# Kernel tuning notes

Hardware: AMD Instinct MI355X
Metric: run time of the kernel (lower is better)

## Reference

```python
import jax, jax.numpy as jnp
import numpy as np

N = 100000      # total nodes across batch of graphs
E = 1600000     # total edges (avg degree 16)
DIN = 16        # raw node feature dim
H = 128         # social_hidden_dim
HEADS = 4
DOUT = H // HEADS
LAYERS = 2
G = 64          # number of graphs in batch
FOUT = 256      # fusion_hidden_dim
NEG_SLOPE = 0.2


def layer_norm(x, g, b, eps=1e-5):
    mu = x.mean(-1, keepdims=True)
    var = ((x - mu) ** 2).mean(-1, keepdims=True)
    return (x - mu) / jnp.sqrt(var + eps) * g + b


def gat_conv(h, src, dst, W, a_src, a_dst, bias):
    # h: [N,H]; src/dst: [E+N] (self-loops included)
    hp = (h @ W).reshape(N, HEADS, DOUT)                    # [N,heads,dout]
    al_s = jnp.einsum('nhd,hd->nh', hp, a_src)              # [N,heads]
    al_d = jnp.einsum('nhd,hd->nh', hp, a_dst)
    logits = jax.nn.leaky_relu(al_s[src] + al_d[dst], NEG_SLOPE)  # [Etot,heads]
    m = jax.ops.segment_max(logits, dst, num_segments=N)    # segment softmax over dst
    e = jnp.exp(logits - m[dst])
    denom = jax.ops.segment_sum(e, dst, num_segments=N)
    alpha = e / (denom[dst] + 1e-16)                        # [Etot,heads]
    msg = hp[src] * alpha[:, :, None]                       # [Etot,heads,dout]
    out = jax.ops.segment_sum(msg, dst, num_segments=N)     # scatter-add
    return out.reshape(N, H) + bias


def setup_inputs():
    key = jax.random.key(0)
    ks = jax.random.split(key, 24)
    s = 0.05
    inp = {
        'x': jax.random.normal(ks[0], (N, DIN), jnp.float32),
        'edge_index': jax.random.randint(ks[1], (2, E), 0, N, jnp.int32),
        'node2graph': (jnp.arange(N, dtype=jnp.int32) * G // N).astype(jnp.int32),
        'Wp': jax.random.normal(ks[2], (DIN, H)) * s,
        'bp': jnp.zeros((H,)),
        'Wq1': jax.random.normal(ks[3], (2 * H, H)) * s,
        'bq1': jnp.zeros((H,)),
        'gq': jnp.ones((H,)), 'beq': jnp.zeros((H,)),
        'Wq2': jax.random.normal(ks[4], (H, FOUT)) * s,
        'bq2': jnp.zeros((FOUT,)),
    }
    for i in range(LAYERS):
        inp[f'Wg{i}'] = jax.random.normal(ks[5 + 4 * i], (H, H)) * s
        inp[f'as{i}'] = jax.random.normal(ks[6 + 4 * i], (HEADS, DOUT)) * s
        inp[f'ad{i}'] = jax.random.normal(ks[7 + 4 * i], (HEADS, DOUT)) * s
        inp[f'bg{i}'] = jnp.zeros((H,))
        inp[f'g{i}'] = jnp.ones((H,))
        inp[f'be{i}'] = jnp.zeros((H,))
    return inp


def reference(x, edge_index, node2graph, Wp, bp, Wq1, bq1, gq, beq, Wq2, bq2,
              Wg0, as0, ad0, bg0, g0, be0, Wg1, as1, ad1, bg1, g1, be1):
    loop = jnp.arange(N, dtype=edge_index.dtype)
    src = jnp.concatenate([edge_index[0], loop])  # add self-loops (PyG default)
    dst = jnp.concatenate([edge_index[1], loop])

    h = jax.nn.gelu(x @ Wp + bp, approximate=False)
    params = [(Wg0, as0, ad0, bg0, g0, be0), (Wg1, as1, ad1, bg1, g1, be1)]
    for (W, a_s, a_d, b, g, be) in params:
        h_new = gat_conv(h, src, dst, W, a_s, a_d, b)
        h = layer_norm(h_new + h, g, be)  # dims match -> residual

    counts = jax.ops.segment_sum(jnp.ones((N, 1), h.dtype), node2graph, num_segments=G)
    mean_pool = jax.ops.segment_sum(h, node2graph, num_segments=G) / jnp.maximum(counts, 1.0)
    max_pool = jax.ops.segment_max(h, node2graph, num_segments=G)
    emb = jnp.concatenate([mean_pool, max_pool], axis=-1)  # [G, 2H]

    p = layer_norm(emb @ Wq1 + bq1, gq, beq)
    p = jax.nn.gelu(p, approximate=False)
    return p @ Wq2 + bq2  # [G, FOUT]
```

## Files before the change

kernel.cpp:

```cpp
#include <hip/hip_runtime.h>

typedef unsigned short u16;
typedef unsigned char u8;
typedef unsigned int u32;
typedef unsigned long long u64;
typedef short short8 __attribute__((ext_vector_type(8)));
typedef float f32x4 __attribute__((ext_vector_type(4)));
typedef float f32x2 __attribute__((ext_vector_type(2)));

#define NN   100000
#define EE   1600000
#define ETOT (EE + NN)
#define NG   64
#define WSTR 136
#define SCANB 98
#define NB   98
#define BCAP 24576
#define OCAP 262144
#define EPB  4096

constexpr size_t AL256(size_t x) { return (x + 255) & ~(size_t)255; }
constexpr size_t OFF_FLAG   = 0;
constexpr size_t OFF_BSUM   = AL256(OFF_FLAG + 256);
constexpr size_t OFF_BCNT   = AL256(OFF_BSUM + 128 * 4);
constexpr size_t OFF_ROWPTR = AL256(OFF_BCNT + 128 * 4);
constexpr size_t OFF_DEG    = AL256(OFF_ROWPTR + (size_t)(NN + 1) * 4);
constexpr size_t OFF_COL    = AL256(OFF_DEG + (size_t)NN * 4);
constexpr size_t OFF_ALS    = AL256(OFF_COL + (size_t)ETOT * 4);
constexpr size_t OFF_ALD    = AL256(OFF_ALS + (size_t)NN * 4 * 4);
constexpr size_t OFF_GSUM   = AL256(OFF_ALD + (size_t)NN * 4 * 4);
constexpr size_t OFF_GKEY   = AL256(OFF_GSUM + (size_t)NG * 128 * 4);
constexpr size_t OFF_GCNT   = AL256(OFF_GKEY + (size_t)NG * 128 * 4);
constexpr size_t OFF_H      = AL256(OFF_GCNT + (size_t)NG * 4);
constexpr size_t OFF_HPB    = AL256(OFF_H + (size_t)NN * 128 * 2);
constexpr size_t OFF_EBUF   = AL256(OFF_HPB + (size_t)NN * 128 * 1);
constexpr size_t OFF_OBUF   = AL256(OFF_EBUF + (size_t)NB * BCAP * 4);
constexpr size_t WS_TOTAL   = AL256(OFF_OBUF + (size_t)OCAP * 8);

__device__ u64 g_ws[WS_TOTAL / 8];

__device__ __forceinline__ char* wsp() { return (char*)g_ws; }
#define WS_FLAG   ((int*)(wsp() + OFF_FLAG))
#define WS_BSUM   ((int*)(wsp() + OFF_BSUM))
#define WS_BCNT   ((int*)(wsp() + OFF_BCNT))
#define WS_ROWPTR ((int*)(wsp() + OFF_ROWPTR))
#define WS_DEG    ((int*)(wsp() + OFF_DEG))
#define WS_COL    ((int*)(wsp() + OFF_COL))
#define WS_ALS    ((float*)(wsp() + OFF_ALS))
#define WS_ALD    ((float*)(wsp() + OFF_ALD))
#define WS_GSUM   ((float*)(wsp() + OFF_GSUM))
#define WS_GKEY   ((u32*)(wsp() + OFF_GKEY))
#define WS_GCNT   ((int*)(wsp() + OFF_GCNT))
#define WS_H      ((u16*)(wsp() + OFF_H))
#define WS_HPB    ((u8*)(wsp() + OFF_HPB))
#define WS_EBUF   ((u32*)(wsp() + OFF_EBUF))
#define WS_OBUF   ((u64*)(wsp() + OFF_OBUF))

__device__ __forceinline__ float b2f(u16 u) { return __uint_as_float(((u32)u) << 16); }
__device__ __forceinline__ float b2f_lo(u32 u) { return __uint_as_float(u << 16); }
__device__ __forceinline__ float b2f_hi(u32 u) { return __uint_as_float(u & 0xffff0000u); }
__device__ __forceinline__ u16 f2bf(float f) {
    u32 u = __float_as_uint(f);
    return (u16)((u + 0x7fffu + ((u >> 16) & 1u)) >> 16);
}
__device__ __forceinline__ float ldf(const void* p, int i, int bf) {
    return bf ? b2f(((const u16*)p)[i]) : ((const float*)p)[i];
}
__device__ __forceinline__ int ldint(const int* p, long long i, int wide) {
    return wide ? p[i * 2] : p[(size_t)i];
}
__device__ __forceinline__ u32 fkey(float f) {
    u32 u = __float_as_uint(f);
    return (u >> 31) ? ~u : (u | 0x80000000u);
}
__device__ __forceinline__ float funkey(u32 k) {
    u32 u = (k & 0x80000000u) ? (k & 0x7fffffffu) : ~k;
    return __uint_as_float(u);
}

__global__ __launch_bounds__(256) void k_zero(const void* __restrict__ x,
                                              const int* __restrict__ ei) {
    if (blockIdx.x == 0 && threadIdx.x < 64) {
        int t = threadIdx.x;
        const u16* p = (const u16*)x;
        u16 u = p[t * 2];
        int e = (u >> 7) & 0xff;
        int ok = ((u & 0x7fffu) == 0) || (e >= 0x60 && e <= 0x9f);
        u64 m1 = __ballot(ok);
        int z = (ei[t * 2 + 1] == 0);
        u64 m2 = __ballot(z);
        if (t == 0) {
            WS_FLAG[0] = (__popcll(m1) >= 48) ? 1 : 0;
            WS_FLAG[1] = (__popcll(m2) >= 56) ? 1 : 0;
        }
    }
    if (blockIdx.x == 0 && threadIdx.x == 64) WS_FLAG[2] = 0;
    int i = blockIdx.x * 256 + threadIdx.x;
    if (i < NN) WS_DEG[i] = 0;
    if (i < NG * 128) { WS_GSUM[i] = 0.f; WS_GKEY[i] = 0u; }
    if (i < NG) WS_GCNT[i] = 0;
    if (i < NB) WS_BCNT[i] = 0;
}

__global__ __launch_bounds__(256) void k_bucket(const int* __restrict__ ei) {
    __shared__ int lcnt[NB], lbase[NB], lcur[NB];
    int t = threadIdx.x;
    int wide = WS_FLAG[1];
    for (int i = t; i < NB; i += 256) { lcnt[i] = 0; lcur[i] = 0; }
    __syncthreads();
    int e0 = blockIdx.x * EPB + t;
    int sA[16], dA[16];
#pragma unroll
    for (int j = 0; j < 16; j++) {
        int e = e0 + j * 256;
        int s = -1, d = 0;
        if (e < ETOT) {
            if (e < EE) {
                if (wide) { s = ((const int2*)ei)[e].x; d = ((const int2*)ei)[(size_t)EE + e].x; }
                else      { s = ei[e];                  d = ei[(size_t)EE + e]; }
            } else { s = e - EE; d = s; }
            if ((u32)s >= NN || (u32)d >= NN) s = -1;
        }
        sA[j] = s; dA[j] = d;
        if (s >= 0) atomicAdd(&lcnt[d >> 10], 1);
    }
    __syncthreads();
    for (int i = t; i < NB; i += 256)
        lbase[i] = atomicAdd(&WS_BCNT[i], lcnt[i]);
    __syncthreads();
    u32* ebuf = WS_EBUF;
#pragma unroll
    for (int j = 0; j < 16; j++) {
        int s = sA[j], d = dA[j];
        if (s < 0) continue;
        int b = d >> 10;
        int r = atomicAdd(&lcur[b], 1);
        int slot = lbase[b] + r;
        if (slot < BCAP) {
            ebuf[(size_t)b * BCAP + slot] = ((u32)(d & 1023) << 17) | (u32)s;
        } else {
            int o = atomicAdd(&WS_FLAG[2], 1);
            if (o < OCAP) {
                WS_OBUF[o] = ((u64)(u32)d << 32) | (u32)s;
                atomicAdd(&WS_DEG[d], 1);
            }
        }
    }
}

__global__ __launch_bounds__(1024) void k_scan1() {
    __shared__ int hist[1024];
    __shared__ int wsum[16];
    int b = blockIdx.x, t = threadIdx.x;
    hist[t] = 0;
    __syncthreads();
    int bc = WS_BCNT[b]; if (bc > BCAP) bc = BCAP;
    const u32* eb = WS_EBUF + (size_t)b * BCAP;
    for (int i = t; i < bc; i += 1024)
        atomicAdd(&hist[eb[i] >> 17], 1);
    __syncthreads();
    int i = b * 1024 + t;
    int v = (i < NN) ? (WS_DEG[i] + hist[t]) : 0;
    int lane = t & 63, wv = t >> 6;
    int x = v;
#pragma unroll
    for (int off = 1; off < 64; off <<= 1) {
        int y = __shfl_up(x, off);
        if (lane >= off) x += y;
    }
    if (lane == 63) wsum[wv] = x;
    __syncthreads();
    if (wv == 0 && lane < 16) {
        int y = wsum[lane];
#pragma unroll
        for (int off = 1; off < 16; off <<= 1) {
            int z = __shfl_up(y, off);
            if (lane >= off) y += z;
        }
        wsum[lane] = y;
    }
    __syncthreads();
    int incl = x + (wv > 0 ? wsum[wv - 1] : 0);
    if (i < NN) WS_ROWPTR[i] = incl - v;
    if (t == 1023) WS_BSUM[b] = incl;
}

__global__ __launch_bounds__(256) void k_place() {
    __shared__ int cur[1024];
    __shared__ int sb[128];
    __shared__ int w0tot;
    int b = blockIdx.x, t = threadIdx.x;
    int lane = t & 63;
    if (t < 128) {
        int x = (t < SCANB) ? WS_BSUM[t] : 0;
#pragma unroll
        for (int off = 1; off < 64; off <<= 1) {
            int y = __shfl_up(x, off);
            if (lane >= off) x += y;
        }
        if (t == 63) w0tot = x;
        sb[t] = x;
    }
    __syncthreads();
    if (t >= 64 && t < 128) sb[t] += w0tot;
    __syncthreads();
    int add = (b > 0) ? sb[b - 1] : 0;
    int n0 = b << 10;
    for (int i = t; i < 1024; i += 256) {
        int n = n0 + i;
        int r = 0;
        if (n < NN) {
            r = WS_ROWPTR[n] + add;
            WS_ROWPTR[n] = r;
        }
        cur[i] = r;
    }
    if (b == 0 && t == 0) WS_ROWPTR[NN] = sb[127];
    __syncthreads();
    int bc = WS_BCNT[b]; if (bc > BCAP) bc = BCAP;
    const u32* eb = WS_EBUF + (size_t)b * BCAP;
    for (int i = t; i < bc; i += 256) {
        u32 pk = eb[i];
        int dl = pk >> 17, s = (int)(pk & 0x1ffffu);
        int pos = atomicAdd(&cur[dl], 1);
        WS_COL[pos] = s;
    }
    int cnt = WS_FLAG[2]; if (cnt > OCAP) cnt = OCAP;
    for (int i = t; i < cnt; i += 256) {
        u64 pk = WS_OBUF[i];
        int d = (int)(pk >> 32);
        if ((d >> 10) == b) {
            int pos = atomicAdd(&cur[d & 1023], 1);
            WS_COL[pos] = (int)(pk & 0xffffffffu);
        }
    }
}

__global__ __launch_bounds__(128) void k_proj(const void* __restrict__ x,
                                              const void* __restrict__ Wp,
                                              const void* __restrict__ bp) {
    __shared__ float sW[16 * 128];
    int t = threadIdx.x;
    int bf = WS_FLAG[0];
    for (int i = t; i < 16 * 128; i += 128) sW[i] = ldf(Wp, i, bf);
    __syncthreads();
    float bj = ldf(bp, t, bf);
    for (int n = blockIdx.x; n < NN; n += gridDim.x) {
        float acc = bj;
#pragma unroll
        for (int k = 0; k < 16; k++)
            acc = fmaf(ldf(x, n * 16 + k, bf), sW[k * 128 + t], acc);
        float g = 0.5f * acc * (1.0f + erff(acc * 0.70710678118654752f));
        WS_H[(size_t)n * 128 + t] = f2bf(g);
    }
}

__global__ __launch_bounds__(256) void k_gemm(const void* __restrict__ Wg,
                                              const void* __restrict__ a_s,
                                              const void* __restrict__ a_d) {
    __shared__ __align__(16) u16 sWt[128 * WSTR];
    int t = threadIdx.x;
    int bf = WS_FLAG[0];
    for (int idx = t; idx < 128 * 128; idx += 256) {
        int k = idx >> 7, n = idx & 127;
        sWt[n * WSTR + k] = bf ? ((const u16*)Wg)[idx] : f2bf(((const float*)Wg)[idx]);
    }
    __syncthreads();
    int wv = t >> 6, lane = t & 63;
    int n0 = wv * 32;
    int quad = lane >> 4, m16 = lane & 15;
    int ce = n0 + 2 * m16;
    float as0v = ldf(a_s, ce, bf),     as1v = ldf(a_s, ce + 1, bf);
    float ad0v = ldf(a_d, ce, bf),     ad1v = ldf(a_d, ce + 1, bf);
    short8 bfr[2][4];
#pragma unroll
    for (int nt = 0; nt < 2; nt++) {
        int n = ce + nt;
#pragma unroll
        for (int ks = 0; ks < 4; ks++)
            bfr[nt][ks] = *(const short8*)&sWt[n * WSTR + ks * 32 + quad * 8];
    }
    u8* hp = WS_HPB;
    const u16* hsrc = WS_H;
    for (int m0 = blockIdx.x * 16; m0 < NN; m0 += gridDim.x * 16) {
        const u16* arow = &hsrc[(size_t)(m0 + m16) * 128];
        f32x4 acc0 = {0.f, 0.f, 0.f, 0.f};
        f32x4 acc1 = {0.f, 0.f, 0.f, 0.f};
#pragma unroll
        for (int ks = 0; ks < 4; ks++) {
            short8 af = *(const short8*)&arow[ks * 32 + quad * 8];
            acc0 = __builtin_amdgcn_mfma_f32_16x16x32_bf16(af, bfr[0][ks], acc0, 0, 0, 0);
            acc1 = __builtin_amdgcn_mfma_f32_16x16x32_bf16(af, bfr[1][ks], acc1, 0, 0, 0);
        }
#pragma unroll
        for (int r = 0; r < 4; r++) {
            size_t row = (size_t)(m0 + quad * 4 + r) * 128;
            u32 pk8 = (u32)__builtin_amdgcn_cvt_pk_fp8_f32(acc0[r], acc1[r], 0, false);
            *(u16*)&hp[row + ce] = (u16)(pk8 & 0xffffu);
            float ps = acc0[r] * as0v + acc1[r] * as1v;
            float pd = acc0[r] * ad0v + acc1[r] * ad1v;
#pragma unroll
            for (int m = 1; m <= 8; m <<= 1) {
                ps += __shfl_xor(ps, m);
                pd += __shfl_xor(pd, m);
            }
            if (m16 == 0) {
                int nrow = m0 + quad * 4 + r;
                WS_ALS[nrow * 4 + wv] = ps;
                WS_ALD[nrow * 4 + wv] = pd;
            }
        }
    }
}

__global__ __launch_bounds__(512) void k_gat(const void* __restrict__ bg,
                                             const void* __restrict__ gam,
                                             const void* __restrict__ bet) {
    int wid = threadIdx.x >> 6, lane = threadIdx.x & 63;
    int n = blockIdx.x * 8 + wid;
    if (n >= NN) return;
    int bf = WS_FLAG[0];
    const int* col = WS_COL;
    const float* als = WS_ALS;
    int k0 = WS_ROWPTR[n], deg = WS_ROWPTR[n + 1] - k0;
    int hd = lane >> 4, eo = lane & 15;
    float aldh = WS_ALD[n * 4 + hd];
    const u16* hp16 = (const u16*)WS_HPB;
    u32* h32 = (u32*)WS_H;
    u32 hv = h32[(size_t)n * 64 + lane];
    int base48 = lane & 48;

    int i0 = eo, i1 = eo + 16;
    int e0 = k0 + (i0 < deg ? i0 : 0);
    int e1 = k0 + (i1 < deg ? i1 : 0);
    int sc0 = col[e0];
    int sc1 = col[e1];
    float v0 = als[sc0 * 4 + hd] + aldh;
    float v1 = als[sc1 * 4 + hd] + aldh;
    v0 = v0 > 0.f ? v0 : 0.2f * v0;
    v1 = v1 > 0.f ? v1 : 0.2f * v1;
    float w0 = (i0 < deg) ? __expf(v0) : 0.f;
    float w1 = (i1 < deg) ? __expf(v1) : 0.f;
    float se = w0 + w1;
    float a0 = 0.f, a1 = 0.f;

#pragma unroll
    for (int j = 0; j < 16; j++) {
        float wj = __shfl(w0, base48 + j);
        int   sj = __builtin_amdgcn_readlane(sc0, j);
        u16 pv = hp16[(size_t)sj * 64 + lane];
        f32x2 mv = __builtin_amdgcn_cvt_pk_f32_fp8((int)pv, false);
        a0 = fmaf(wj, mv.x, a0);
        a1 = fmaf(wj, mv.y, a1);
    }
    if (deg > 16) {
#pragma unroll
        for (int j = 0; j < 16; j++) {
            float wj = __shfl(w1, base48 + j);
            int   sj = __builtin_amdgcn_readlane(sc1, j);
            u16 pv = hp16[(size_t)sj * 64 + lane];
            f32x2 mv = __builtin_amdgcn_cvt_pk_f32_fp8((int)pv, false);
            a0 = fmaf(wj, mv.x, a0);
            a1 = fmaf(wj, mv.y, a1);
        }
    }

    if (__builtin_expect(deg > 32, 0)) {
        for (int c = 32; c < deg; c += 16) {
            int i = c + eo;
            float w = 0.f; int scol = 0;
            if (i < deg) {
                scol = col[k0 + i];
                float v = als[scol * 4 + hd] + aldh;
                v = v > 0.f ? v : 0.2f * v;
                w = __expf(v);
            }
            se += w;
            int rem = deg - c; if (rem > 16) rem = 16;
            for (int j = 0; j < rem; j++) {
                float wj = __shfl(w, base48 + j);
                int sj = __shfl(scol, base48 + j);
                u16 pv = hp16[(size_t)sj * 64 + lane];
                f32x2 mv = __builtin_amdgcn_cvt_pk_f32_fp8((int)pv, false);
                a0 = fmaf(wj, mv.x, a0);
                a1 = fmaf(wj, mv.y, a1);
            }
        }
    }

    se += __shfl_xor(se, 1);
    se += __shfl_xor(se, 2);
    se += __shfl_xor(se, 4);
    se += __shfl_xor(se, 8);
    float inv = 1.f / (se + 1e-16f);
    int d0 = lane * 2, d1 = d0 + 1;
    float r0 = a0 * inv + ldf(bg, d0, bf) + b2f_lo(hv);
    float r1 = a1 * inv + ldf(bg, d1, bf) + b2f_hi(hv);
    float s1 = r0 + r1;
#pragma unroll
    for (int m = 1; m <= 32; m <<= 1) s1 += __shfl_xor(s1, m);
    float mu = s1 * (1.f / 128.f);
    float e0f = r0 - mu, e1f = r1 - mu;
    float s2 = e0f * e0f + e1f * e1f;
#pragma unroll
    for (int m = 1; m <= 32; m <<= 1) s2 += __shfl_xor(s2, m);
    float rstd = rsqrtf(s2 * (1.f / 128.f) + 1e-5f);
    float y0 = e0f * rstd * ldf(gam, d0, bf) + ldf(bet, d0, bf);
    float y1 = e1f * rstd * ldf(gam, d1, bf) + ldf(bet, d1, bf);
    h32[(size_t)n * 64 + lane] = (u32)f2bf(y0) | ((u32)f2bf(y1) << 16);
}

__global__ __launch_bounds__(128) void k_pool(const int* __restrict__ n2g) {
    int j = threadIdx.x;
    int wide = WS_FLAG[1];
    int n0 = blockIdx.x * 128;
    int n1 = n0 + 128; if (n1 > NN) n1 = NN;
    float runs = 0.f, runm = -3.4e38f;
    int rung = -1, runc = 0;
    for (int n = n0; n < n1; n++) {
        int g = ldint(n2g, n, wide);
        if (g != rung) {
            if (rung >= 0 && (u32)rung < NG) {
                atomicAdd(&WS_GSUM[rung * 128 + j], runs);
                atomicMax(&WS_GKEY[rung * 128 + j], fkey(runm));
                if (j == 0) atomicAdd(&WS_GCNT[rung], runc);
            }
            rung = g; runs = 0.f; runm = -3.4e38f; runc = 0;
        }
        float v = b2f(WS_H[(size_t)n * 128 + j]);
        runs += v;
        runm = fmaxf(runm, v);
        runc++;
    }
    if (rung >= 0 && (u32)rung < NG) {
        atomicAdd(&WS_GSUM[rung * 128 + j], runs);
        atomicMax(&WS_GKEY[rung * 128 + j], fkey(runm));
        if (j == 0) atomicAdd(&WS_GCNT[rung], runc);
    }
}

__global__ __launch_bounds__(256) void k_head(const void* __restrict__ Wq1,
                                              const void* __restrict__ bq1,
                                              const void* __restrict__ gq,
                                              const void* __restrict__ beq,
                                              const void* __restrict__ Wq2,
                                              const void* __restrict__ bq2,
                                              float* __restrict__ out) {
    __shared__ float sem[256];
    __shared__ float sp[128];
    __shared__ float red[4];
    int g = blockIdx.x, t = threadIdx.x;
    int bf = WS_FLAG[0];
    float cnt = fmaxf((float)WS_GCNT[g], 1.f);
    if (t < 128) sem[t] = WS_GSUM[g * 128 + t] / cnt;
    else         sem[t] = funkey(WS_GKEY[g * 128 + (t - 128)]);
    __syncthreads();
    float a = 0.f;
    if (t < 128) {
        a = ldf(bq1, t, bf);
        for (int k = 0; k < 256; k++) a = fmaf(sem[k], ldf(Wq1, k * 128 + t, bf), a);
    }
    int lane = t & 63, wv = t >> 6;
    float s1 = (t < 128) ? a : 0.f;
#pragma unroll
    for (int m = 1; m <= 32; m <<= 1) s1 += __shfl_xor(s1, m);
    if (lane == 0) red[wv] = s1;
    __syncthreads();
    float mu = (red[0] + red[1]) * (1.f / 128.f);
    float d = (t < 128) ? (a - mu) : 0.f;
    float s2 = d * d;
#pragma unroll
    for (int m = 1; m <= 32; m <<= 1) s2 += __shfl_xor(s2, m);
    __syncthreads();
    if (lane == 0) red[wv] = s2;
    __syncthreads();
    float var = (red[0] + red[1]) * (1.f / 128.f);
    if (t < 128) {
        float p = d * rsqrtf(var + 1e-5f) * ldf(gq, t, bf) + ldf(beq, t, bf);
        sp[t] = 0.5f * p * (1.0f + erff(p * 0.70710678118654752f));
    }
    __syncthreads();
    float o = ldf(bq2, t, bf);
    for (int k = 0; k < 128; k++)
        o = fmaf(sp[k], ldf(Wq2, k * 256 + t, bf), o);
    out[g * 256 + t] = o;
}

extern "C" void kernel_launch(void* const* d_in, const int* in_sizes, int n_in,
                              void* d_out, int out_size, void* d_ws, size_t ws_size,
                              hipStream_t stream) {
    const void* x   = d_in[0];
    const int* ei   = (const int*)d_in[1];
    const int* n2g  = (const int*)d_in[2];
    const void* Wp  = d_in[3];
    const void* bp  = d_in[4];
    const void* Wq1 = d_in[5];
    const void* bq1 = d_in[6];
    const void* gq  = d_in[7];
    const void* beq = d_in[8];
    const void* Wq2 = d_in[9];
    const void* bq2 = d_in[10];
    const void* Wg0 = d_in[11];
    const void* as0 = d_in[12];
    const void* ad0 = d_in[13];
    const void* bg0 = d_in[14];
    const void* g0  = d_in[15];
    const void* be0 = d_in[16];
    const void* Wg1 = d_in[17];
    const void* as1 = d_in[18];
    const void* ad1 = d_in[19];
    const void* bg1 = d_in[20];
    const void* g1  = d_in[21];
    const void* be1 = d_in[22];
    (void)d_ws; (void)ws_size; (void)in_sizes; (void)n_in; (void)out_size;

    k_zero<<<(NN + 255) / 256, 256, 0, stream>>>(x, ei);

    k_bucket<<<(ETOT + EPB - 1) / EPB, 256, 0, stream>>>(ei);
    k_scan1<<<SCANB, 1024, 0, stream>>>();
    k_place<<<NB, 256, 0, stream>>>();

    k_proj<<<2048, 128, 0, stream>>>(x, Wp, bp);

    k_gemm<<<2048, 256, 0, stream>>>(Wg0, as0, ad0);
    k_gat<<<(NN + 7) / 8, 512, 0, stream>>>(bg0, g0, be0);
    k_gemm<<<2048, 256, 0, stream>>>(Wg1, as1, ad1);
    k_gat<<<(NN + 7) / 8, 512, 0, stream>>>(bg1, g1, be1);

    k_pool<<<(NN + 127) / 128, 128, 0, stream>>>(n2g);
    k_head<<<NG, 256, 0, stream>>>(Wq1, bq1, gq, beq, Wq2, bq2, (float*)d_out);
}
```

Baseline: 551.4 us.

## Handle self-loops inline, merge scan/place kernels, stage GEMM rows in LDS

Self-loop edges are no longer inserted into the CSR. Each GAT node computes its own self-attention weight and message directly, which shrinks the edge bucketing and column array. The separate scan and place kernels are merged into one 1024-thread kernel that derives each bucket's global offset from the bucket counts plus per-bucket overflow counts, removing one launch and the rowptr rewrite pass. The GEMM now stages 16 rows of h through LDS with coalesced loads and runs with half the grid. These add barriers and shared memory per GEMM tile, and the overflow accounting path gains an extra atomic.

```diff
diff --git a/kernel.cpp b/kernel.cpp
--- a/kernel.cpp
+++ b/kernel.cpp
@@ -10,10 +10,8 @@
 
 #define NN   100000
 #define EE   1600000
-#define ETOT (EE + NN)
 #define NG   64
 #define WSTR 136
-#define SCANB 98
 #define NB   98
 #define BCAP 24576
 #define OCAP 262144
@@ -21,12 +19,12 @@
 
 constexpr size_t AL256(size_t x) { return (x + 255) & ~(size_t)255; }
 constexpr size_t OFF_FLAG   = 0;
-constexpr size_t OFF_BSUM   = AL256(OFF_FLAG + 256);
-constexpr size_t OFF_BCNT   = AL256(OFF_BSUM + 128 * 4);
+constexpr size_t OFF_OCNT   = AL256(OFF_FLAG + 256);
+constexpr size_t OFF_BCNT   = AL256(OFF_OCNT + 128 * 4);
 constexpr size_t OFF_ROWPTR = AL256(OFF_BCNT + 128 * 4);
 constexpr size_t OFF_DEG    = AL256(OFF_ROWPTR + (size_t)(NN + 1) * 4);
 constexpr size_t OFF_COL    = AL256(OFF_DEG + (size_t)NN * 4);
-constexpr size_t OFF_ALS    = AL256(OFF_COL + (size_t)ETOT * 4);
+constexpr size_t OFF_ALS    = AL256(OFF_COL + (size_t)(EE + 1024) * 4);
 constexpr size_t OFF_ALD    = AL256(OFF_ALS + (size_t)NN * 4 * 4);
 constexpr size_t OFF_GSUM   = AL256(OFF_ALD + (size_t)NN * 4 * 4);
 constexpr size_t OFF_GKEY   = AL256(OFF_GSUM + (size_t)NG * 128 * 4);
@@ -41,7 +39,7 @@
 
 __device__ __forceinline__ char* wsp() { return (char*)g_ws; }
 #define WS_FLAG   ((int*)(wsp() + OFF_FLAG))
-#define WS_BSUM   ((int*)(wsp() + OFF_BSUM))
+#define WS_OCNT   ((int*)(wsp() + OFF_OCNT))
 #define WS_BCNT   ((int*)(wsp() + OFF_BCNT))
 #define WS_ROWPTR ((int*)(wsp() + OFF_ROWPTR))
 #define WS_DEG    ((int*)(wsp() + OFF_DEG))
@@ -99,7 +97,7 @@
     if (i < NN) WS_DEG[i] = 0;
     if (i < NG * 128) { WS_GSUM[i] = 0.f; WS_GKEY[i] = 0u; }
     if (i < NG) WS_GCNT[i] = 0;
-    if (i < NB) WS_BCNT[i] = 0;
+    if (i < NB) { WS_BCNT[i] = 0; WS_OCNT[i] = 0; }
 }
 
 __global__ __launch_bounds__(256) void k_bucket(const int* __restrict__ ei) {
@@ -114,11 +112,9 @@
     for (int j = 0; j < 16; j++) {
         int e = e0 + j * 256;
         int s = -1, d = 0;
-        if (e < ETOT) {
-            if (e < EE) {
-                if (wide) { s = ((const int2*)ei)[e].x; d = ((const int2*)ei)[(size_t)EE + e].x; }
-                else      { s = ei[e];                  d = ei[(size_t)EE + e]; }
-            } else { s = e - EE; d = s; }
+        if (e < EE) {
+            if (wide) { s = ((const int2*)ei)[e].x; d = ((const int2*)ei)[(size_t)EE + e].x; }
+            else      { s = ei[e];                  d = ei[(size_t)EE + e]; }
             if ((u32)s >= NN || (u32)d >= NN) s = -1;
         }
         sA[j] = s; dA[j] = d;
@@ -143,25 +139,47 @@
             if (o < OCAP) {
                 WS_OBUF[o] = ((u64)(u32)d << 32) | (u32)s;
                 atomicAdd(&WS_DEG[d], 1);
+                atomicAdd(&WS_OCNT[d >> 10], 1);
             }
         }
     }
 }
 
-__global__ __launch_bounds__(1024) void k_scan1() {
+__global__ __launch_bounds__(1024) void k_place() {
     __shared__ int hist[1024];
+    __shared__ int sb[128];
     __shared__ int wsum[16];
+    __shared__ int w0tot;
     int b = blockIdx.x, t = threadIdx.x;
+    int lane = t & 63, wv = t >> 6;
     hist[t] = 0;
-    __syncthreads();
+    if (t < 128) {
+        int c = 0;
+        if (t < NB) {
+            c = WS_BCNT[t]; if (c > BCAP) c = BCAP;
+            c += WS_OCNT[t];
+        }
+        int x = c;
+#pragma unroll
+        for (int off = 1; off < 64; off <<= 1) {
+            int y = __shfl_up(x, off);
+            if (lane >= off) x += y;
+        }
+        if (t == 63) w0tot = x;
+        sb[t] = x;
+    }
+    __syncthreads();
+    if (t >= 64 && t < 128) sb[t] += w0tot;
+    __syncthreads();
+    int base = (b > 0) ? sb[b - 1] : 0;
+    if (b == 0 && t == 0) WS_ROWPTR[NN] = sb[NB - 1];
     int bc = WS_BCNT[b]; if (bc > BCAP) bc = BCAP;
     const u32* eb = WS_EBUF + (size_t)b * BCAP;
     for (int i = t; i < bc; i += 1024)
         atomicAdd(&hist[eb[i] >> 17], 1);
     __syncthreads();
-    int i = b * 1024 + t;
-    int v = (i < NN) ? (WS_DEG[i] + hist[t]) : 0;
-    int lane = t & 63, wv = t >> 6;
+    int n = (b << 10) + t;
+    int v = (n < NN) ? (hist[t] + WS_DEG[n]) : 0;
     int x = v;
 #pragma unroll
     for (int off = 1; off < 64; off <<= 1) {
@@ -180,57 +198,22 @@
         wsum[lane] = y;
     }
     __syncthreads();
-    int incl = x + (wv > 0 ? wsum[wv - 1] : 0);
-    if (i < NN) WS_ROWPTR[i] = incl - v;
-    if (t == 1023) WS_BSUM[b] = incl;
-}
-
-__global__ __launch_bounds__(256) void k_place() {
-    __shared__ int cur[1024];
-    __shared__ int sb[128];
-    __shared__ int w0tot;
-    int b = blockIdx.x, t = threadIdx.x;
-    int lane = t & 63;
-    if (t < 128) {
-        int x = (t < SCANB) ? WS_BSUM[t] : 0;
-#pragma unroll
-        for (int off = 1; off < 64; off <<= 1) {
-            int y = __shfl_up(x, off);
-            if (lane >= off) x += y;
-        }
-        if (t == 63) w0tot = x;
-        sb[t] = x;
-    }
-    __syncthreads();
-    if (t >= 64 && t < 128) sb[t] += w0tot;
-    __syncthreads();
-    int add = (b > 0) ? sb[b - 1] : 0;
-    int n0 = b << 10;
-    for (int i = t; i < 1024; i += 256) {
-        int n = n0 + i;
-        int r = 0;
-        if (n < NN) {
-            r = WS_ROWPTR[n] + add;
-            WS_ROWPTR[n] = r;
-        }
-        cur[i] = r;
-    }
-    if (b == 0 && t == 0) WS_ROWPTR[NN] = sb[127];
-    __syncthreads();
-    int bc = WS_BCNT[b]; if (bc > BCAP) bc = BCAP;
-    const u32* eb = WS_EBUF + (size_t)b * BCAP;
-    for (int i = t; i < bc; i += 256) {
+    int r = base + x + (wv > 0 ? wsum[wv - 1] : 0) - v;
+    if (n < NN) WS_ROWPTR[n] = r;
+    __syncthreads();
+    hist[t] = r;
+    __syncthreads();
+    for (int i = t; i < bc; i += 1024) {
         u32 pk = eb[i];
-        int dl = pk >> 17, s = (int)(pk & 0x1ffffu);
-        int pos = atomicAdd(&cur[dl], 1);
-        WS_COL[pos] = s;
+        int pos = atomicAdd(&hist[pk >> 17], 1);
+        WS_COL[pos] = (int)(pk & 0x1ffffu);
     }
     int cnt = WS_FLAG[2]; if (cnt > OCAP) cnt = OCAP;
-    for (int i = t; i < cnt; i += 256) {
+    for (int i = t; i < cnt; i += 1024) {
         u64 pk = WS_OBUF[i];
         int d = (int)(pk >> 32);
         if ((d >> 10) == b) {
-            int pos = atomicAdd(&cur[d & 1023], 1);
+            int pos = atomicAdd(&hist[d & 1023], 1);
             WS_COL[pos] = (int)(pk & 0xffffffffu);
         }
     }
@@ -259,6 +242,7 @@
                                               const void* __restrict__ a_s,
                                               const void* __restrict__ a_d) {
     __shared__ __align__(16) u16 sWt[128 * WSTR];
+    __shared__ __align__(16) u16 sH[16 * WSTR];
     int t = threadIdx.x;
     int bf = WS_FLAG[0];
     for (int idx = t; idx < 128 * 128; idx += 256) {
@@ -281,14 +265,20 @@
             bfr[nt][ks] = *(const short8*)&sWt[n * WSTR + ks * 32 + quad * 8];
     }
     u8* hp = WS_HPB;
-    const u16* hsrc = WS_H;
+    const u32* h32 = (const u32*)WS_H;
+    u32* sH32 = (u32*)sH;
     for (int m0 = blockIdx.x * 16; m0 < NN; m0 += gridDim.x * 16) {
-        const u16* arow = &hsrc[(size_t)(m0 + m16) * 128];
+        __syncthreads();
+        for (int idx = t; idx < 16 * 64; idx += 256) {
+            int r = idx >> 6, c2 = idx & 63;
+            sH32[r * 68 + c2] = h32[(size_t)(m0 + r) * 64 + c2];
+        }
+        __syncthreads();
         f32x4 acc0 = {0.f, 0.f, 0.f, 0.f};
         f32x4 acc1 = {0.f, 0.f, 0.f, 0.f};
 #pragma unroll
         for (int ks = 0; ks < 4; ks++) {
-            short8 af = *(const short8*)&arow[ks * 32 + quad * 8];
+            short8 af = *(const short8*)&sH[m16 * WSTR + ks * 32 + quad * 8];
             acc0 = __builtin_amdgcn_mfma_f32_16x16x32_bf16(af, bfr[0][ks], acc0, 0, 0, 0);
             acc1 = __builtin_amdgcn_mfma_f32_16x16x32_bf16(af, bfr[1][ks], acc1, 0, 0, 0);
         }
@@ -328,13 +318,20 @@
     const u16* hp16 = (const u16*)WS_HPB;
     u32* h32 = (u32*)WS_H;
     u32 hv = h32[(size_t)n * 64 + lane];
+    u16 pvs = hp16[(size_t)n * 64 + lane];
     int base48 = lane & 48;
+
+    float vs = als[n * 4 + hd] + aldh;
+    vs = vs > 0.f ? vs : 0.2f * vs;
+    float wself = __expf(vs);
 
     int i0 = eo, i1 = eo + 16;
     int e0 = k0 + (i0 < deg ? i0 : 0);
     int e1 = k0 + (i1 < deg ? i1 : 0);
     int sc0 = col[e0];
     int sc1 = col[e1];
+    if ((u32)sc0 >= NN) sc0 = 0;
+    if ((u32)sc1 >= NN) sc1 = 0;
     float v0 = als[sc0 * 4 + hd] + aldh;
     float v1 = als[sc1 * 4 + hd] + aldh;
     v0 = v0 > 0.f ? v0 : 0.2f * v0;
@@ -342,7 +339,8 @@
     float w0 = (i0 < deg) ? __expf(v0) : 0.f;
     float w1 = (i1 < deg) ? __expf(v1) : 0.f;
     float se = w0 + w1;
-    float a0 = 0.f, a1 = 0.f;
+    f32x2 mvs = __builtin_amdgcn_cvt_pk_f32_fp8((int)pvs, false);
+    float a0 = wself * mvs.x, a1 = wself * mvs.y;
 
 #pragma unroll
     for (int j = 0; j < 16; j++) {
@@ -392,6 +390,7 @@
     se += __shfl_xor(se, 2);
     se += __shfl_xor(se, 4);
     se += __shfl_xor(se, 8);
+    se += wself;
     float inv = 1.f / (se + 1e-16f);
     int d0 = lane * 2, d1 = d0 + 1;
     float r0 = a0 * inv + ldf(bg, d0, bf) + b2f_lo(hv);
@@ -516,15 +515,14 @@
 
     k_zero<<<(NN + 255) / 256, 256, 0, stream>>>(x, ei);
 
-    k_bucket<<<(ETOT + EPB - 1) / EPB, 256, 0, stream>>>(ei);
-    k_scan1<<<SCANB, 1024, 0, stream>>>();
-    k_place<<<NB, 256, 0, stream>>>();
+    k_bucket<<<(EE + EPB - 1) / EPB, 256, 0, stream>>>(ei);
+    k_place<<<NB, 1024, 0, stream>>>();
 
     k_proj<<<2048, 128, 0, stream>>>(x, Wp, bp);
 
-    k_gemm<<<2048, 256, 0, stream>>>(Wg0, as0, ad0);
+    k_gemm<<<1024, 256, 0, stream>>>(Wg0, as0, ad0);
     k_gat<<<(NN + 7) / 8, 512, 0, stream>>>(bg0, g0, be0);
-    k_gemm<<<2048, 256, 0, stream>>>(Wg1, as1, ad1);
+    k_gemm<<<1024, 256, 0, stream>>>(Wg1, as1, ad1);
     k_gat<<<(NN + 7) / 8, 512, 0, stream>>>(bg1, g1, be1);
 
     k_pool<<<(NN + 127) / 128, 128, 0, stream>>>(n2g);
```

Result: faster. 519.3 us (-5.8%).
